# Kernel tuning notes

Hardware: AMD Instinct MI355X
Metric: run time of the kernel (lower is better)

## Reference

```python
import jax, jax.numpy as jnp
import numpy as np

B, IN, H = 4096, 1024, 1024


def setup_inputs() -> dict:
    key = jax.random.key(0)
    ks = jax.random.split(key, 12)
    s = float(np.sqrt(6.0 / (IN + H)))  # xavier-uniform-like scale
    u = lambda k, shp: jax.random.uniform(k, shp, jnp.float32, -s, s)
    return {
        "x": jax.random.normal(ks[0], (B, IN), jnp.float32),
        "h_prev": jax.random.normal(ks[1], (B, H), jnp.float32),
        "c_prev": jax.random.normal(ks[2], (B, H), jnp.float32),
        "n_prev": jnp.ones((B, H), jnp.float32),
        "m_prev": jnp.zeros((B, H), jnp.float32),
        "Wi_x": u(ks[3], (H, IN)), "bi": jnp.zeros((H,), jnp.float32), "Wi_h": u(ks[4], (H, H)),
        "Wf_x": u(ks[5], (H, IN)), "bf": jnp.full((H,), 2.0, jnp.float32), "Wf_h": u(ks[6], (H, H)),
        "Wz_x": u(ks[7], (H, IN)), "bz": jnp.zeros((H,), jnp.float32), "Wz_h": u(ks[8], (H, H)),
        "Wo_x": u(ks[9], (H, IN)), "bo": jnp.zeros((H,), jnp.float32), "Wo_h": u(ks[10], (H, H)),
    }


def reference(x, h_prev, c_prev, n_prev, m_prev,
              Wi_x, bi, Wi_h, Wf_x, bf, Wf_h,
              Wz_x, bz, Wz_h, Wo_x, bo, Wo_h):
    # 8 projections (x-side with bias, h-side without), torch Linear: y = x @ W.T + b
    i_tilde = x @ Wi_x.T + bi + h_prev @ Wi_h.T
    f_aff   = x @ Wf_x.T + bf + h_prev @ Wf_h.T
    z_aff   = x @ Wz_x.T + bz + h_prev @ Wz_h.T
    o_aff   = x @ Wo_x.T + bo + h_prev @ Wo_h.T

    # forget_as_exp=False path: sigmoid forget gate, log-domain stabilizer
    log_f = jnp.log(jnp.clip(jax.nn.sigmoid(f_aff), 1e-8, None))
    m_t = jnp.maximum(log_f + m_prev, i_tilde)
    i_prime = jnp.exp(i_tilde - m_t)
    f_prime = jnp.exp(log_f + m_prev - m_t)

    z = jnp.tanh(z_aff)
    c_t = f_prime * c_prev + i_prime * z
    n_t = f_prime * n_prev + i_prime
    h_t = jax.nn.sigmoid(o_aff) * (c_t / jnp.clip(n_t, 1e-6, None))
    return h_t, c_t, n_t, m_t
```

## Files before the change

### kernel.cpp

```cpp
#include <hip/hip_runtime.h>
#include <stdint.h>


#define B_DIM 4096
#define K_DIM 2048
#define TM 128
#define TN 128
#define BK 32

typedef __bf16 bf16x8 __attribute__((ext_vector_type(8)));
typedef float f32x4 __attribute__((ext_vector_type(4)));
typedef unsigned short ushort8 __attribute__((ext_vector_type(8)));

__device__ __forceinline__ unsigned short f2bf(float f) {
  unsigned u = __float_as_uint(f);
  u += 0x7fffu + ((u >> 16) & 1u);
  return (unsigned short)(u >> 16);
}
__device__ __forceinline__ float bf2f(unsigned short u) {
  return __uint_as_float(((unsigned)u) << 16);
}

__device__ __forceinline__ void load_lds16(const void* g, void* lds) {
  __builtin_amdgcn_global_load_lds(
      (const __attribute__((address_space(1))) unsigned int*)(uintptr_t)g,
      (__attribute__((address_space(3))) unsigned int*)(unsigned int)(uintptr_t)lds,
      16, 0, 0);
}

__device__ __forceinline__ ushort8 load8_as_bf16(const void* base, size_t off, bool isbf) {
  if (isbf) return *(const ushort8*)((const unsigned short*)base + off);
  const float* f = (const float*)base + off;
  float4 v0 = ((const float4*)f)[0];
  float4 v1 = ((const float4*)f)[1];
  ushort8 o;
  o[0] = f2bf(v0.x); o[1] = f2bf(v0.y); o[2] = f2bf(v0.z); o[3] = f2bf(v0.w);
  o[4] = f2bf(v1.x); o[5] = f2bf(v1.y); o[6] = f2bf(v1.z); o[7] = f2bf(v1.w);
  return o;
}

__global__ void pack_all(const void* __restrict__ xv, const void* __restrict__ hv,
                         const void* __restrict__ Wix, const void* __restrict__ Wih,
                         const void* __restrict__ Wfx, const void* __restrict__ Wfh,
                         const void* __restrict__ Wzx, const void* __restrict__ Wzh,
                         const void* __restrict__ Wox, const void* __restrict__ Woh,
                         unsigned short* __restrict__ Apk, unsigned short* __restrict__ Bpk) {
  const int blk = blockIdx.x;
  const int lane = threadIdx.x & 63;
  const bool isA = blk < 4096;
  const unsigned* disc = (const unsigned*)(isA ? xv : Wix);
  int v = 0;
  if (lane < 32) {
    unsigned e = (disc[lane] >> 7) & 0xFFu;
    v = (e > (isA ? 129u : 122u)) ? 1 : 0;
  }
  const bool isbf = (__ballot(v) == 0ull);

  if (isA) {
    int t = blk * 256 + threadIdx.x;
    int base = t * 8;
    int m = base >> 11;
    int k = base & 2047;
    size_t off = (size_t)m * 1024 + (k & 1023);
    const void* src = (k < 1024) ? xv : hv;
    *(ushort8*)(Apk + base) = load8_as_bf16(src, off, isbf);
  } else {
    int t = (blk - 4096) * 256 + threadIdx.x;
    int base = t * 8;
    int p = base >> 11;
    int k = base & 2047;
    int g = (p >> 4) & 3;
    int n = ((p >> 6) << 4) | (p & 15);
    const void* W;
    if (k < 1024) W = (g == 0) ? Wix : (g == 1) ? Wfx : (g == 2) ? Wzx : Wox;
    else          W = (g == 0) ? Wih : (g == 1) ? Wfh : (g == 2) ? Wzh : Woh;
    size_t off = (size_t)n * 1024 + (k & 1023);
    *(ushort8*)(Bpk + base) = load8_as_bf16(W, off, isbf);
  }
}

__global__ __launch_bounds__(256) void gemm_fused(
    const unsigned short* __restrict__ Apk,
    const unsigned short* __restrict__ Bpk,
    const void* __restrict__ bi, const void* __restrict__ bfg,
    const void* __restrict__ bz, const void* __restrict__ bo,
    const void* __restrict__ c_prev, const void* __restrict__ n_prev,
    const void* __restrict__ m_prev,
    float* __restrict__ out)
{
  __shared__ unsigned short As[2][TM * BK];
  __shared__ unsigned short Bs[2][TN * BK];

  const int tid  = threadIdx.x;
  const int wave = tid >> 6;
  const int lane = tid & 63;
  const int wr = wave >> 1;
  const int wc = wave & 1;
  const int qrow = lane >> 4;
  const int col  = lane & 15;

  const int m0 = blockIdx.x * TM;
  const int p0 = blockIdx.y * TN;

  f32x4 acc[4][4] = {};

  const int swz = ((qrow + (col >> 1)) & 3) * 8;

#define STAGE(k0, buf)                                                        \
  {                                                                           \
    _Pragma("unroll")                                                         \
    for (int q = 0; q < 2; ++q) {                                             \
      int c = wave * 128 + q * 64 + lane;                                     \
      int row = c >> 2;                                                       \
      int cb = ((c & 3) - (row >> 1)) & 3;                                    \
      const unsigned short* gA = Apk + (size_t)(m0 + row) * K_DIM + (k0) + cb * 8; \
      const unsigned short* gB = Bpk + (size_t)(p0 + row) * K_DIM + (k0) + cb * 8; \
      load_lds16(gA, (void*)(As[buf] + (wave * 128 + q * 64) * 8));           \
      load_lds16(gB, (void*)(Bs[buf] + (wave * 128 + q * 64) * 8));           \
    }                                                                         \
  }

  STAGE(0, 0);
  __syncthreads();

  int cur = 0;
  for (int k0 = 0; k0 < K_DIM; k0 += BK, cur ^= 1) {
    if (k0 + BK < K_DIM) STAGE(k0 + BK, cur ^ 1);

    bf16x8 af[4], bfr[4];
#pragma unroll
    for (int t = 0; t < 4; ++t) {
      af[t]  = *(const bf16x8*)(As[cur] + (wr * 64 + t * 16 + col) * BK + swz);
      bfr[t] = *(const bf16x8*)(Bs[cur] + (wc * 64 + t * 16 + col) * BK + swz);
    }
#pragma unroll
    for (int ti = 0; ti < 4; ++ti)
#pragma unroll
      for (int tj = 0; tj < 4; ++tj)
        acc[ti][tj] = __builtin_amdgcn_mfma_f32_16x16x32_bf16(af[ti], bfr[tj], acc[ti][tj], 0, 0, 0);

    __syncthreads();
  }

  const bool sbf = (((const unsigned*)n_prev)[0] == 0x3F803F80u);
  const bool bbf = (((const unsigned*)bfg)[0]    == 0x40004000u);
  const int n = (blockIdx.y * 2 + wc) * 16 + col;
  const float bi_n = bbf ? bf2f(((const unsigned short*)bi)[n])  : ((const float*)bi)[n];
  const float bf_n = bbf ? bf2f(((const unsigned short*)bfg)[n]) : ((const float*)bfg)[n];
  const float bz_n = bbf ? bf2f(((const unsigned short*)bz)[n])  : ((const float*)bz)[n];
  const float bo_n = bbf ? bf2f(((const unsigned short*)bo)[n])  : ((const float*)bo)[n];
  const int rowbase = m0 + wr * 64 + qrow * 4;

  float* out_h = out;
  float* out_c = out + 4194304;
  float* out_n = out + 2 * 4194304;
  float* out_m = out + 3 * 4194304;

#pragma unroll
  for (int ti = 0; ti < 4; ++ti) {
#pragma unroll
    for (int r = 0; r < 4; ++r) {
      int row = rowbase + ti * 16 + r;
      int idx = row * 1024 + n;
      float it = acc[ti][0][r] + bi_n;
      float fa = acc[ti][1][r] + bf_n;
      float za = acc[ti][2][r] + bz_n;
      float oa = acc[ti][3][r] + bo_n;
      float cp  = sbf ? bf2f(((const unsigned short*)c_prev)[idx]) : ((const float*)c_prev)[idx];
      float npv = sbf ? bf2f(((const unsigned short*)n_prev)[idx]) : ((const float*)n_prev)[idx];
      float mp  = sbf ? bf2f(((const unsigned short*)m_prev)[idx]) : ((const float*)m_prev)[idx];

      float sf = 1.f / (1.f + __expf(-fa));
      sf = fmaxf(sf, 1e-8f);
      float lf = __logf(sf);
      float mt = fmaxf(lf + mp, it);
      float ip = __expf(it - mt);
      float fp = __expf(lf + mp - mt);
      float zc = fminf(fmaxf(za, -15.f), 15.f);
      float e2 = __expf(2.f * zc);
      float z  = (e2 - 1.f) / (e2 + 1.f);
      float ct = fp * cp + ip * z;
      float nt = fp * npv + ip;
      float so = 1.f / (1.f + __expf(-oa));
      float ht = so * (ct / fmaxf(nt, 1e-6f));

      out_h[idx] = ht;
      out_c[idx] = ct;
      out_n[idx] = nt;
      out_m[idx] = mt;
    }
  }
}

extern "C" void kernel_launch(void* const* d_in, const int* in_sizes, int n_in,
                              void* d_out, int out_size, void* d_ws, size_t ws_size,
                              hipStream_t stream) {
  const void* x      = d_in[0];
  const void* h_prev = d_in[1];
  const void* c_prev = d_in[2];
  const void* n_prev = d_in[3];
  const void* m_prev = d_in[4];
  const void* Wi_x = d_in[5];
  const void* bi   = d_in[6];
  const void* Wi_h = d_in[7];
  const void* Wf_x = d_in[8];
  const void* bf   = d_in[9];
  const void* Wf_h = d_in[10];
  const void* Wz_x = d_in[11];
  const void* bz   = d_in[12];
  const void* Wz_h = d_in[13];
  const void* Wo_x = d_in[14];
  const void* bo   = d_in[15];
  const void* Wo_h = d_in[16];

  unsigned short* Apk = (unsigned short*)d_ws;
  unsigned short* Bpk = Apk + (size_t)B_DIM * K_DIM;

  pack_all<<<8192, 256, 0, stream>>>(x, h_prev, Wi_x, Wi_h, Wf_x, Wf_h,
                                     Wz_x, Wz_h, Wo_x, Wo_h, Apk, Bpk);
  dim3 grid(B_DIM / TM, 4096 / TN);
  gemm_fused<<<grid, 256, 0, stream>>>(Apk, Bpk, bi, bf, bz, bo,
                                       c_prev, n_prev, m_prev,
                                       (float*)d_out);
}
```

Baseline: 293.6 us.

## Pack operands in MFMA fragment order and load fragments directly from global memory

The pack kernel now writes A and B in a tiled layout that matches the MFMA fragment order (16-row groups, 32-wide K tiles, 64 lanes × 8 elements). The GEMM drops LDS staging and barriers and has each wave load its fragments straight from global memory, with register double-buffering of the next K tile. The grid is flattened to 1024 blocks. This removes LDS traffic and synchronisation, but tiles shared by waves are no longer reused through LDS, so each wave fetches its own data and the kernel depends more on L2 bandwidth and latency hiding.

After: 280.7 us. 4.4% less time.

```diff
diff --git a/kernel.cpp b/kernel.cpp
--- a/kernel.cpp
+++ b/kernel.cpp
@@ -4,9 +4,6 @@
 
 #define B_DIM 4096
 #define K_DIM 2048
-#define TM 128
-#define TN 128
-#define BK 32
 
 typedef __bf16 bf16x8 __attribute__((ext_vector_type(8)));
 typedef float f32x4 __attribute__((ext_vector_type(4)));
@@ -19,13 +16,6 @@
 }
 __device__ __forceinline__ float bf2f(unsigned short u) {
   return __uint_as_float(((unsigned)u) << 16);
-}
-
-__device__ __forceinline__ void load_lds16(const void* g, void* lds) {
-  __builtin_amdgcn_global_load_lds(
-      (const __attribute__((address_space(1))) unsigned int*)(uintptr_t)g,
-      (__attribute__((address_space(3))) unsigned int*)(unsigned int)(uintptr_t)lds,
-      16, 0, 0);
 }
 
 __device__ __forceinline__ ushort8 load8_as_bf16(const void* base, size_t off, bool isbf) {
@@ -56,26 +46,26 @@
   }
   const bool isbf = (__ballot(v) == 0ull);
 
+  const int t = (isA ? blk : blk - 4096) * 256 + threadIdx.x;
+  const int cl = t & 63;
+  const int kt = (t >> 6) & 63;
+  const int x16 = t >> 12;
+  const int lr = cl & 15;
+  const int k = kt * 32 + (cl >> 4) * 8;
+
   if (isA) {
-    int t = blk * 256 + threadIdx.x;
-    int base = t * 8;
-    int m = base >> 11;
-    int k = base & 2047;
+    int m = x16 * 16 + lr;
+    const void* src = (k < 1024) ? xv : hv;
     size_t off = (size_t)m * 1024 + (k & 1023);
-    const void* src = (k < 1024) ? xv : hv;
-    *(ushort8*)(Apk + base) = load8_as_bf16(src, off, isbf);
+    *(ushort8*)(Apk + (size_t)t * 8) = load8_as_bf16(src, off, isbf);
   } else {
-    int t = (blk - 4096) * 256 + threadIdx.x;
-    int base = t * 8;
-    int p = base >> 11;
-    int k = base & 2047;
-    int g = (p >> 4) & 3;
-    int n = ((p >> 6) << 4) | (p & 15);
+    int g = x16 & 3;
+    int n = (x16 >> 2) * 16 + lr;
     const void* W;
     if (k < 1024) W = (g == 0) ? Wix : (g == 1) ? Wfx : (g == 2) ? Wzx : Wox;
     else          W = (g == 0) ? Wih : (g == 1) ? Wfh : (g == 2) ? Wzh : Woh;
     size_t off = (size_t)n * 1024 + (k & 1023);
-    *(ushort8*)(Bpk + base) = load8_as_bf16(W, off, isbf);
+    *(ushort8*)(Bpk + (size_t)t * 8) = load8_as_bf16(W, off, isbf);
   }
 }
 
@@ -88,68 +78,62 @@
     const void* __restrict__ m_prev,
     float* __restrict__ out)
 {
-  __shared__ unsigned short As[2][TM * BK];
-  __shared__ unsigned short Bs[2][TN * BK];
-
   const int tid  = threadIdx.x;
   const int wave = tid >> 6;
   const int lane = tid & 63;
-  const int wr = wave >> 1;
-  const int wc = wave & 1;
   const int qrow = lane >> 4;
   const int col  = lane & 15;
 
-  const int m0 = blockIdx.x * TM;
-  const int p0 = blockIdx.y * TN;
+  const int bx  = blockIdx.x;
+  const int mb  = bx & 31;
+  const int qb2 = bx >> 5;
+  const int wr = wave >> 1, wc = wave & 1;
+  const int m64 = mb * 2 + wr;
+  const int q   = qb2 * 2 + wc;
+
+  const unsigned short* pa = Apk + (size_t)(m64 * 4) * 32768 + lane * 8;
+  const unsigned short* pb = Bpk + (size_t)(q * 4)   * 32768 + lane * 8;
 
   f32x4 acc[4][4] = {};
-
-  const int swz = ((qrow + (col >> 1)) & 3) * 8;
-
-#define STAGE(k0, buf)                                                        \
-  {                                                                           \
-    _Pragma("unroll")                                                         \
-    for (int q = 0; q < 2; ++q) {                                             \
-      int c = wave * 128 + q * 64 + lane;                                     \
-      int row = c >> 2;                                                       \
-      int cb = ((c & 3) - (row >> 1)) & 3;                                    \
-      const unsigned short* gA = Apk + (size_t)(m0 + row) * K_DIM + (k0) + cb * 8; \
-      const unsigned short* gB = Bpk + (size_t)(p0 + row) * K_DIM + (k0) + cb * 8; \
-      load_lds16(gA, (void*)(As[buf] + (wave * 128 + q * 64) * 8));           \
-      load_lds16(gB, (void*)(Bs[buf] + (wave * 128 + q * 64) * 8));           \
-    }                                                                         \
-  }
-
-  STAGE(0, 0);
-  __syncthreads();
-
-  int cur = 0;
-  for (int k0 = 0; k0 < K_DIM; k0 += BK, cur ^= 1) {
-    if (k0 + BK < K_DIM) STAGE(k0 + BK, cur ^ 1);
-
-    bf16x8 af[4], bfr[4];
+  bf16x8 a_cur[4], b_cur[4];
+
+#pragma unroll
+  for (int t = 0; t < 4; ++t) {
+    a_cur[t] = *(const bf16x8*)(pa + t * 32768);
+    b_cur[t] = *(const bf16x8*)(pb + t * 32768);
+  }
+
+  for (int kt = 0; kt < 63; ++kt) {
+    bf16x8 a_nxt[4], b_nxt[4];
+    const unsigned short* pan = pa + (kt + 1) * 512;
+    const unsigned short* pbn = pb + (kt + 1) * 512;
 #pragma unroll
     for (int t = 0; t < 4; ++t) {
-      af[t]  = *(const bf16x8*)(As[cur] + (wr * 64 + t * 16 + col) * BK + swz);
-      bfr[t] = *(const bf16x8*)(Bs[cur] + (wc * 64 + t * 16 + col) * BK + swz);
+      a_nxt[t] = *(const bf16x8*)(pan + t * 32768);
+      b_nxt[t] = *(const bf16x8*)(pbn + t * 32768);
     }
 #pragma unroll
     for (int ti = 0; ti < 4; ++ti)
 #pragma unroll
       for (int tj = 0; tj < 4; ++tj)
-        acc[ti][tj] = __builtin_amdgcn_mfma_f32_16x16x32_bf16(af[ti], bfr[tj], acc[ti][tj], 0, 0, 0);
-
-    __syncthreads();
-  }
+        acc[ti][tj] = __builtin_amdgcn_mfma_f32_16x16x32_bf16(a_cur[ti], b_cur[tj], acc[ti][tj], 0, 0, 0);
+#pragma unroll
+    for (int t = 0; t < 4; ++t) { a_cur[t] = a_nxt[t]; b_cur[t] = b_nxt[t]; }
+  }
+#pragma unroll
+  for (int ti = 0; ti < 4; ++ti)
+#pragma unroll
+    for (int tj = 0; tj < 4; ++tj)
+      acc[ti][tj] = __builtin_amdgcn_mfma_f32_16x16x32_bf16(a_cur[ti], b_cur[tj], acc[ti][tj], 0, 0, 0);
 
   const bool sbf = (((const unsigned*)n_prev)[0] == 0x3F803F80u);
   const bool bbf = (((const unsigned*)bfg)[0]    == 0x40004000u);
-  const int n = (blockIdx.y * 2 + wc) * 16 + col;
+  const int n = q * 16 + col;
   const float bi_n = bbf ? bf2f(((const unsigned short*)bi)[n])  : ((const float*)bi)[n];
   const float bf_n = bbf ? bf2f(((const unsigned short*)bfg)[n]) : ((const float*)bfg)[n];
   const float bz_n = bbf ? bf2f(((const unsigned short*)bz)[n])  : ((const float*)bz)[n];
   const float bo_n = bbf ? bf2f(((const unsigned short*)bo)[n])  : ((const float*)bo)[n];
-  const int rowbase = m0 + wr * 64 + qrow * 4;
+  const int rowbase = m64 * 64 + qrow * 4;
 
   float* out_h = out;
   float* out_c = out + 4194304;
@@ -218,8 +202,7 @@
 
   pack_all<<<8192, 256, 0, stream>>>(x, h_prev, Wi_x, Wi_h, Wf_x, Wf_h,
                                      Wz_x, Wz_h, Wo_x, Wo_h, Apk, Bpk);
-  dim3 grid(B_DIM / TM, 4096 / TN);
-  gemm_fused<<<grid, 256, 0, stream>>>(Apk, Bpk, bi, bf, bz, bo,
+  gemm_fused<<<1024, 256, 0, stream>>>(Apk, Bpk, bi, bf, bz, bo,
                                        c_prev, n_prev, m_prev,
                                        (float*)d_out);
 }
```
